# Kernel tuning notes

Hardware: AMD Instinct MI355X
Metric: run time of the kernel (lower is better)

Reference implementation:

```python
import jax, jax.numpy as jnp
import numpy as np

N_NODES = 50000
N_EDGES = 600000
D_IN = 128
D_HID = 128


def _sage_conv(x, src, dst, W_l, b_l, W_r):
    """PyG SAGEConv (mean aggr): out = lin_l(mean_{j in N(i)} x_j) + lin_r(x_i).
    bias lives in lin_l only."""
    n = x.shape[0]
    agg = jax.ops.segment_sum(x[src], dst, num_segments=n)            # [N, D]
    cnt = jax.ops.segment_sum(jnp.ones((src.shape[0],), x.dtype), dst, num_segments=n)
    mean = agg / jnp.maximum(cnt, 1.0)[:, None]
    return mean @ W_l.T + b_l + x @ W_r.T


def setup_inputs() -> dict:
    key = jax.random.key(0)
    ks = jax.random.split(key, 8)
    glorot = lambda k, o, i: jax.random.normal(k, (o, i), jnp.float32) * np.sqrt(2.0 / (o + i))
    return {
        "x": jax.random.normal(ks[0], (N_NODES, D_IN), jnp.float32),
        "edge_index": jax.random.randint(ks[1], (2, N_EDGES), 0, N_NODES, jnp.int64),
        "W1_l": glorot(ks[2], D_HID, D_IN),
        "b1": jnp.zeros((D_HID,), jnp.float32),
        "W1_r": glorot(ks[3], D_HID, D_IN),
        "W2_l": glorot(ks[4], D_HID, D_HID),
        "b2": jnp.zeros((D_HID,), jnp.float32),
        "W2_r": glorot(ks[5], D_HID, D_HID),
    }


def reference(x, edge_index, W1_l, b1, W1_r, W2_l, b2, W2_r):
    src, dst = edge_index[0], edge_index[1]
    h = _sage_conv(x, src, dst, W1_l, b1, W1_r)
    h = jax.nn.leaky_relu(h, negative_slope=0.2)
    return _sage_conv(h, src, dst, W2_l, b2, W2_r)
```

## Files before the change

kernel.cpp:

```cpp
#include <hip/hip_runtime.h>

#define N_NODES 50000
#define N_EDGES 600000
#define D 128
#define SCAN_BLOCKS ((N_NODES + 255) / 256)

typedef __attribute__((ext_vector_type(8))) short bf16x8;
typedef __attribute__((ext_vector_type(4))) float floatx4;

__device__ inline unsigned int f2bf(float f) {
    unsigned int u = __float_as_uint(f);
    return (u + 0x7FFFu + ((u >> 16) & 1u)) >> 16;
}
__device__ inline float bf_lo(unsigned int u) { return __uint_as_float(u << 16); }
__device__ inline float bf_hi(unsigned int u) { return __uint_as_float(u & 0xFFFF0000u); }

__global__ void k_prep(const float* __restrict__ x, unsigned short* __restrict__ xbf,
                       const float* __restrict__ wa, const float* __restrict__ wb,
                       const float* __restrict__ wc, const float* __restrict__ wd,
                       unsigned short* __restrict__ wbf,
                       const int* __restrict__ dst, int* __restrict__ cnt) {
    const int b = blockIdx.x;
    const int t = threadIdx.x;
    if (b < 6250) {
        int i = b * 256 + t;
        float4 v = ((const float4*)x)[i];
        uint2 o;
        o.x = f2bf(v.x) | (f2bf(v.y) << 16);
        o.y = f2bf(v.z) | (f2bf(v.w) << 16);
        ((uint2*)xbf)[i] = o;
    } else if (b < 6506) {
        int i = (b - 6250) * 256 + t;
        const float* srcs[4] = {wa, wb, wc, wd};
        wbf[i] = (unsigned short)f2bf(srcs[i >> 14][i & 16383]);
    } else {
        int e = (b - 6506) * 256 + t;
        if (e < N_EDGES) atomicAdd(&cnt[dst[e]], 1);
    }
}


__global__ void k_scan1(const int* __restrict__ cnt, int* __restrict__ off,
                        int* __restrict__ partial) {
    __shared__ int sdata[256];
    const int t = threadIdx.x;
    const int i = blockIdx.x * 256 + t;
    int v = (i < N_NODES) ? cnt[i] : 0;
    sdata[t] = v;
    __syncthreads();
    for (int d = 1; d < 256; d <<= 1) {
        int u = (t >= d) ? sdata[t - d] : 0;
        __syncthreads();
        sdata[t] += u;
        __syncthreads();
    }
    if (i < N_NODES) off[i] = sdata[t] - v;
    if (t == 255) partial[blockIdx.x] = sdata[255];
}

__global__ void k_scan2(int* __restrict__ partial) {
    __shared__ int sdata[256];
    const int t = threadIdx.x;
    int v = (t < SCAN_BLOCKS) ? partial[t] : 0;
    sdata[t] = v;
    __syncthreads();
    for (int d = 1; d < 256; d <<= 1) {
        int u = (t >= d) ? sdata[t - d] : 0;
        __syncthreads();
        sdata[t] += u;
        __syncthreads();
    }
    if (t < SCAN_BLOCKS) partial[t] = sdata[t] - v;
}

__global__ void k_scan3(int* __restrict__ off, const int* __restrict__ partial,
                        int* __restrict__ cursor) {
    const int i = blockIdx.x * 256 + threadIdx.x;
    if (i < N_NODES) {
        int o = off[i] + partial[blockIdx.x];
        off[i] = o;
        cursor[i] = o;
    }
    if (i == 0) off[N_NODES] = N_EDGES;
}

__global__ void k_bucket(const int* __restrict__ src, const int* __restrict__ dst,
                         int* __restrict__ cursor, int* __restrict__ ebuf) {
    int e = blockIdx.x * blockDim.x + threadIdx.x;
    if (e < N_EDGES) {
        int p = atomicAdd(&cursor[dst[e]], 1);
        ebuf[p] = src[e];
    }
}

template <bool RELU, bool OUT_BF16>
__global__ void __launch_bounds__(256) k_gather_layer(
    const int* __restrict__ off, const int* __restrict__ ebuf,
    const unsigned short* __restrict__ Xbf,
    const unsigned short* __restrict__ Wlbf, const float* __restrict__ bias,
    const unsigned short* __restrict__ Wrbf, void* __restrict__ outp) {
    __shared__ unsigned short tile[16][136];

    const int t = threadIdx.x;
    const int node0 = blockIdx.x * 16;

    {
        const int nl = t >> 4, q = t & 15;
        const int node = node0 + nl;
        int s0 = off[node], s1 = off[node + 1];
        float acc[8] = {0.f, 0.f, 0.f, 0.f, 0.f, 0.f, 0.f, 0.f};
        int e = s0;
        for (; e + 4 <= s1; e += 4) {
            int sa = ebuf[e], sb = ebuf[e + 1], sc = ebuf[e + 2], sd = ebuf[e + 3];
            uint4 va = *(const uint4*)(Xbf + (size_t)sa * D + q * 8);
            uint4 vb = *(const uint4*)(Xbf + (size_t)sb * D + q * 8);
            uint4 vc = *(const uint4*)(Xbf + (size_t)sc * D + q * 8);
            uint4 vd = *(const uint4*)(Xbf + (size_t)sd * D + q * 8);
            acc[0] += bf_lo(va.x) + bf_lo(vb.x) + bf_lo(vc.x) + bf_lo(vd.x);
            acc[1] += bf_hi(va.x) + bf_hi(vb.x) + bf_hi(vc.x) + bf_hi(vd.x);
            acc[2] += bf_lo(va.y) + bf_lo(vb.y) + bf_lo(vc.y) + bf_lo(vd.y);
            acc[3] += bf_hi(va.y) + bf_hi(vb.y) + bf_hi(vc.y) + bf_hi(vd.y);
            acc[4] += bf_lo(va.z) + bf_lo(vb.z) + bf_lo(vc.z) + bf_lo(vd.z);
            acc[5] += bf_hi(va.z) + bf_hi(vb.z) + bf_hi(vc.z) + bf_hi(vd.z);
            acc[6] += bf_lo(va.w) + bf_lo(vb.w) + bf_lo(vc.w) + bf_lo(vd.w);
            acc[7] += bf_hi(va.w) + bf_hi(vb.w) + bf_hi(vc.w) + bf_hi(vd.w);
        }
        for (; e < s1; ++e) {
            int sa = ebuf[e];
            uint4 va = *(const uint4*)(Xbf + (size_t)sa * D + q * 8);
            acc[0] += bf_lo(va.x); acc[1] += bf_hi(va.x);
            acc[2] += bf_lo(va.y); acc[3] += bf_hi(va.y);
            acc[4] += bf_lo(va.z); acc[5] += bf_hi(va.z);
            acc[6] += bf_lo(va.w); acc[7] += bf_hi(va.w);
        }
        float inv = (s1 > s0) ? 1.0f / (float)(s1 - s0) : 0.0f;
        uint4 o;
        o.x = f2bf(acc[0] * inv) | (f2bf(acc[1] * inv) << 16);
        o.y = f2bf(acc[2] * inv) | (f2bf(acc[3] * inv) << 16);
        o.z = f2bf(acc[4] * inv) | (f2bf(acc[5] * inv) << 16);
        o.w = f2bf(acc[6] * inv) | (f2bf(acc[7] * inv) << 16);
        *(uint4*)(&tile[nl][q * 8]) = o;
    }
    __syncthreads();

    const int lane = t & 63;
    const int wv = t >> 6;
    const int l15 = lane & 15;
    const int quad = lane >> 4;

    floatx4 c0 = (floatx4)(0.f), c1 = (floatx4)(0.f);
    const int nf0 = wv * 2, nf1 = wv * 2 + 1;

    const unsigned short* mrow = &tile[l15][quad * 8];
    const unsigned short* arowX = Xbf + (size_t)(node0 + l15) * D + quad * 8;

#pragma unroll
    for (int kk = 0; kk < 4; ++kk) {
        bf16x8 a = *(const bf16x8*)(mrow + kk * 32);
        bf16x8 b0 = *(const bf16x8*)(Wlbf + (size_t)(nf0 * 16 + l15) * D + kk * 32 + quad * 8);
        bf16x8 b1 = *(const bf16x8*)(Wlbf + (size_t)(nf1 * 16 + l15) * D + kk * 32 + quad * 8);
        c0 = __builtin_amdgcn_mfma_f32_16x16x32_bf16(a, b0, c0, 0, 0, 0);
        c1 = __builtin_amdgcn_mfma_f32_16x16x32_bf16(a, b1, c1, 0, 0, 0);
    }
#pragma unroll
    for (int kk = 0; kk < 4; ++kk) {
        bf16x8 a = *(const bf16x8*)(arowX + kk * 32);
        bf16x8 b0 = *(const bf16x8*)(Wrbf + (size_t)(nf0 * 16 + l15) * D + kk * 32 + quad * 8);
        bf16x8 b1 = *(const bf16x8*)(Wrbf + (size_t)(nf1 * 16 + l15) * D + kk * 32 + quad * 8);
        c0 = __builtin_amdgcn_mfma_f32_16x16x32_bf16(a, b0, c0, 0, 0, 0);
        c1 = __builtin_amdgcn_mfma_f32_16x16x32_bf16(a, b1, c1, 0, 0, 0);
    }

#pragma unroll
    for (int j = 0; j < 2; ++j) {
        floatx4 c = j ? c1 : c0;
        int f = (wv * 2 + j) * 16 + l15;
        float bv = bias[f];
#pragma unroll
        for (int r = 0; r < 4; ++r) {
            float v = c[r] + bv;
            if (RELU) v = v > 0.f ? v : 0.2f * v;
            int node = node0 + quad * 4 + r;
            if (OUT_BF16)
                ((unsigned short*)outp)[(size_t)node * D + f] = (unsigned short)f2bf(v);
            else
                ((float*)outp)[(size_t)node * D + f] = v;
        }
    }
}


extern "C" void kernel_launch(void* const* d_in, const int* in_sizes, int n_in,
                              void* d_out, int out_size, void* d_ws, size_t ws_size,
                              hipStream_t stream) {
    (void)in_sizes; (void)n_in; (void)out_size; (void)ws_size;

    const float* x   = (const float*)d_in[0];
    const int*   ei  = (const int*)d_in[1];
    const float* W1l = (const float*)d_in[2];
    const float* b1  = (const float*)d_in[3];
    const float* W1r = (const float*)d_in[4];
    const float* W2l = (const float*)d_in[5];
    const float* b2  = (const float*)d_in[6];
    const float* W2r = (const float*)d_in[7];

    const int* src = ei;
    const int* dst = ei + N_EDGES;

    char* ws = (char*)d_ws;
    int*   cnt     = (int*)(ws + 0);
    int*   off     = (int*)(ws + 200064);
    int*   cursor  = (int*)(ws + 400128);
    int*   partial = (int*)(ws + 600192);
    int*   ebuf    = (int*)(ws + 601216);
    unsigned short* wbf = (unsigned short*)(ws + 3001216);
    unsigned short* xbf = (unsigned short*)(ws + 3132288);
    unsigned short* hbf = (unsigned short*)(ws + 15932288);
    float* out = (float*)d_out;

    unsigned short* w1l_bf = wbf;
    unsigned short* w1r_bf = wbf + 16384;
    unsigned short* w2l_bf = wbf + 32768;
    unsigned short* w2r_bf = wbf + 49152;

    hipMemsetAsync(cnt, 0, N_NODES * sizeof(int), stream);
    k_prep<<<8850, 256, 0, stream>>>(x, xbf, W1l, W1r, W2l, W2r, wbf, dst, cnt);
    k_scan1<<<SCAN_BLOCKS, 256, 0, stream>>>(cnt, off, partial);
    k_scan2<<<1, 256, 0, stream>>>(partial);
    k_scan3<<<SCAN_BLOCKS, 256, 0, stream>>>(off, partial, cursor);
    k_bucket<<<(N_EDGES + 255) / 256, 256, 0, stream>>>(src, dst, cursor, ebuf);

    k_gather_layer<true, true><<<N_NODES / 16, 256, 0, stream>>>(
        off, ebuf, xbf, w1l_bf, b1, w1r_bf, (void*)hbf);
    k_gather_layer<false, false><<<N_NODES / 16, 256, 0, stream>>>(
        off, ebuf, hbf, w2l_bf, b2, w2r_bf, (void*)out);
}
```

Before: 251.8 us.

## Replace CSR scan/bucket build with fixed-capacity per-node neighbor lists

Drops the three scan kernels and the bucket kernel. The prep kernel now does a single atomic pass per edge that places each source id into a per-node slot array of capacity 64, stored as 16-bit indices. Edges past the capacity go to a global spill list, which the gather kernel scans linearly only for overflowing nodes. The gather loop is unrolled to 8 loads in flight, and the bf16 copy of x now lives in the output buffer to save workspace. This removes several kernel launches and the serial scan dependency. In exchange it relies on node ids fitting in 16 bits, and the spill path would be slow if many nodes had high degree.

```diff
diff --git a/kernel.cpp b/kernel.cpp
--- a/kernel.cpp
+++ b/kernel.cpp
@@ -3,7 +3,7 @@
 #define N_NODES 50000
 #define N_EDGES 600000
 #define D 128
-#define SCAN_BLOCKS ((N_NODES + 255) / 256)
+#define CAP 64
 
 typedef __attribute__((ext_vector_type(8))) short bf16x8;
 typedef __attribute__((ext_vector_type(4))) float floatx4;
@@ -19,83 +19,49 @@
                        const float* __restrict__ wa, const float* __restrict__ wb,
                        const float* __restrict__ wc, const float* __restrict__ wd,
                        unsigned short* __restrict__ wbf,
-                       const int* __restrict__ dst, int* __restrict__ cnt) {
+                       const int* __restrict__ src, const int* __restrict__ dst,
+                       int* __restrict__ cnt, unsigned short* __restrict__ buf,
+                       int* __restrict__ spillN, int* __restrict__ spillD,
+                       int* __restrict__ spillS) {
     const int b = blockIdx.x;
     const int t = threadIdx.x;
-    if (b < 6250) {
-        int i = b * 256 + t;
+    if (b < 2344) {
+        int e = b * 256 + t;
+        if (e < N_EDGES) {
+            int d = dst[e], s = src[e];
+            int p = atomicAdd(&cnt[d], 1);
+            if (p < CAP) {
+                buf[(size_t)d * CAP + p] = (unsigned short)s;
+            } else {
+                int k = atomicAdd(spillN, 1);
+                spillD[k] = d; spillS[k] = s;
+            }
+        }
+    } else if (b < 8594) {
+        int i = (b - 2344) * 256 + t;
         float4 v = ((const float4*)x)[i];
         uint2 o;
         o.x = f2bf(v.x) | (f2bf(v.y) << 16);
         o.y = f2bf(v.z) | (f2bf(v.w) << 16);
         ((uint2*)xbf)[i] = o;
-    } else if (b < 6506) {
-        int i = (b - 6250) * 256 + t;
+    } else {
+        int i = (b - 8594) * 256 + t;
         const float* srcs[4] = {wa, wb, wc, wd};
         wbf[i] = (unsigned short)f2bf(srcs[i >> 14][i & 16383]);
-    } else {
-        int e = (b - 6506) * 256 + t;
-        if (e < N_EDGES) atomicAdd(&cnt[dst[e]], 1);
-    }
-}
-
-
-__global__ void k_scan1(const int* __restrict__ cnt, int* __restrict__ off,
-                        int* __restrict__ partial) {
-    __shared__ int sdata[256];
-    const int t = threadIdx.x;
-    const int i = blockIdx.x * 256 + t;
-    int v = (i < N_NODES) ? cnt[i] : 0;
-    sdata[t] = v;
-    __syncthreads();
-    for (int d = 1; d < 256; d <<= 1) {
-        int u = (t >= d) ? sdata[t - d] : 0;
-        __syncthreads();
-        sdata[t] += u;
-        __syncthreads();
-    }
-    if (i < N_NODES) off[i] = sdata[t] - v;
-    if (t == 255) partial[blockIdx.x] = sdata[255];
-}
-
-__global__ void k_scan2(int* __restrict__ partial) {
-    __shared__ int sdata[256];
-    const int t = threadIdx.x;
-    int v = (t < SCAN_BLOCKS) ? partial[t] : 0;
-    sdata[t] = v;
-    __syncthreads();
-    for (int d = 1; d < 256; d <<= 1) {
-        int u = (t >= d) ? sdata[t - d] : 0;
-        __syncthreads();
-        sdata[t] += u;
-        __syncthreads();
-    }
-    if (t < SCAN_BLOCKS) partial[t] = sdata[t] - v;
-}
-
-__global__ void k_scan3(int* __restrict__ off, const int* __restrict__ partial,
-                        int* __restrict__ cursor) {
-    const int i = blockIdx.x * 256 + threadIdx.x;
-    if (i < N_NODES) {
-        int o = off[i] + partial[blockIdx.x];
-        off[i] = o;
-        cursor[i] = o;
-    }
-    if (i == 0) off[N_NODES] = N_EDGES;
-}
-
-__global__ void k_bucket(const int* __restrict__ src, const int* __restrict__ dst,
-                         int* __restrict__ cursor, int* __restrict__ ebuf) {
-    int e = blockIdx.x * blockDim.x + threadIdx.x;
-    if (e < N_EDGES) {
-        int p = atomicAdd(&cursor[dst[e]], 1);
-        ebuf[p] = src[e];
-    }
-}
+    }
+}
+
+#define ACC8(vv) do { \
+    acc[0] += bf_lo((vv).x); acc[1] += bf_hi((vv).x); \
+    acc[2] += bf_lo((vv).y); acc[3] += bf_hi((vv).y); \
+    acc[4] += bf_lo((vv).z); acc[5] += bf_hi((vv).z); \
+    acc[6] += bf_lo((vv).w); acc[7] += bf_hi((vv).w); } while (0)
 
 template <bool RELU, bool OUT_BF16>
 __global__ void __launch_bounds__(256) k_gather_layer(
-    const int* __restrict__ off, const int* __restrict__ ebuf,
+    const int* __restrict__ cnt, const unsigned short* __restrict__ buf,
+    const int* __restrict__ spillN, const int* __restrict__ spillD,
+    const int* __restrict__ spillS,
     const unsigned short* __restrict__ Xbf,
     const unsigned short* __restrict__ Wlbf, const float* __restrict__ bias,
     const unsigned short* __restrict__ Wrbf, void* __restrict__ outp) {
@@ -107,33 +73,41 @@
     {
         const int nl = t >> 4, q = t & 15;
         const int node = node0 + nl;
-        int s0 = off[node], s1 = off[node + 1];
+        const int deg = cnt[node];
+        const int m = deg < CAP ? deg : CAP;
+        const unsigned short* __restrict__ nb = buf + (size_t)node * CAP;
         float acc[8] = {0.f, 0.f, 0.f, 0.f, 0.f, 0.f, 0.f, 0.f};
-        int e = s0;
-        for (; e + 4 <= s1; e += 4) {
-            int sa = ebuf[e], sb = ebuf[e + 1], sc = ebuf[e + 2], sd = ebuf[e + 3];
-            uint4 va = *(const uint4*)(Xbf + (size_t)sa * D + q * 8);
-            uint4 vb = *(const uint4*)(Xbf + (size_t)sb * D + q * 8);
-            uint4 vc = *(const uint4*)(Xbf + (size_t)sc * D + q * 8);
-            uint4 vd = *(const uint4*)(Xbf + (size_t)sd * D + q * 8);
-            acc[0] += bf_lo(va.x) + bf_lo(vb.x) + bf_lo(vc.x) + bf_lo(vd.x);
-            acc[1] += bf_hi(va.x) + bf_hi(vb.x) + bf_hi(vc.x) + bf_hi(vd.x);
-            acc[2] += bf_lo(va.y) + bf_lo(vb.y) + bf_lo(vc.y) + bf_lo(vd.y);
-            acc[3] += bf_hi(va.y) + bf_hi(vb.y) + bf_hi(vc.y) + bf_hi(vd.y);
-            acc[4] += bf_lo(va.z) + bf_lo(vb.z) + bf_lo(vc.z) + bf_lo(vd.z);
-            acc[5] += bf_hi(va.z) + bf_hi(vb.z) + bf_hi(vc.z) + bf_hi(vd.z);
-            acc[6] += bf_lo(va.w) + bf_lo(vb.w) + bf_lo(vc.w) + bf_lo(vd.w);
-            acc[7] += bf_hi(va.w) + bf_hi(vb.w) + bf_hi(vc.w) + bf_hi(vd.w);
-        }
-        for (; e < s1; ++e) {
-            int sa = ebuf[e];
-            uint4 va = *(const uint4*)(Xbf + (size_t)sa * D + q * 8);
-            acc[0] += bf_lo(va.x); acc[1] += bf_hi(va.x);
-            acc[2] += bf_lo(va.y); acc[3] += bf_hi(va.y);
-            acc[4] += bf_lo(va.z); acc[5] += bf_hi(va.z);
-            acc[6] += bf_lo(va.w); acc[7] += bf_hi(va.w);
-        }
-        float inv = (s1 > s0) ? 1.0f / (float)(s1 - s0) : 0.0f;
+        int e = 0;
+        for (; e + 8 <= m; e += 8) {
+            uint4 v[8];
+#pragma unroll
+            for (int u = 0; u < 8; ++u)
+                v[u] = *(const uint4*)(Xbf + (size_t)nb[e + u] * D + q * 8);
+#pragma unroll
+            for (int u = 0; u < 8; ++u) ACC8(v[u]);
+        }
+        for (; e + 4 <= m; e += 4) {
+            uint4 v[4];
+#pragma unroll
+            for (int u = 0; u < 4; ++u)
+                v[u] = *(const uint4*)(Xbf + (size_t)nb[e + u] * D + q * 8);
+#pragma unroll
+            for (int u = 0; u < 4; ++u) ACC8(v[u]);
+        }
+        for (; e < m; ++e) {
+            uint4 v = *(const uint4*)(Xbf + (size_t)nb[e] * D + q * 8);
+            ACC8(v);
+        }
+        if (deg > CAP) {
+            int sn = *spillN;
+            for (int k = 0; k < sn; ++k) {
+                if (spillD[k] == node) {
+                    uint4 v = *(const uint4*)(Xbf + (size_t)spillS[k] * D + q * 8);
+                    ACC8(v);
+                }
+            }
+        }
+        float inv = (deg > 0) ? 1.0f / (float)deg : 0.0f;
         uint4 o;
         o.x = f2bf(acc[0] * inv) | (f2bf(acc[1] * inv) << 16);
         o.y = f2bf(acc[2] * inv) | (f2bf(acc[3] * inv) << 16);
@@ -208,14 +182,15 @@
     const int* dst = ei + N_EDGES;
 
     char* ws = (char*)d_ws;
-    int*   cnt     = (int*)(ws + 0);
-    int*   off     = (int*)(ws + 200064);
-    int*   cursor  = (int*)(ws + 400128);
-    int*   partial = (int*)(ws + 600192);
-    int*   ebuf    = (int*)(ws + 601216);
-    unsigned short* wbf = (unsigned short*)(ws + 3001216);
-    unsigned short* xbf = (unsigned short*)(ws + 3132288);
-    unsigned short* hbf = (unsigned short*)(ws + 15932288);
+    int* cnt              = (int*)(ws + 0);
+    int* spillN           = (int*)(ws + 200000);
+    int* spillD           = (int*)(ws + 200064);
+    int* spillS           = (int*)(ws + 2600064);
+    unsigned short* buf   = (unsigned short*)(ws + 5000064);
+    unsigned short* wbf   = (unsigned short*)(ws + 11400064);
+    unsigned short* hbf   = (unsigned short*)(ws + 11531136);
+
+    unsigned short* xbf = (unsigned short*)d_out;
     float* out = (float*)d_out;
 
     unsigned short* w1l_bf = wbf;
@@ -223,15 +198,13 @@
     unsigned short* w2l_bf = wbf + 32768;
     unsigned short* w2r_bf = wbf + 49152;
 
-    hipMemsetAsync(cnt, 0, N_NODES * sizeof(int), stream);
-    k_prep<<<8850, 256, 0, stream>>>(x, xbf, W1l, W1r, W2l, W2r, wbf, dst, cnt);
-    k_scan1<<<SCAN_BLOCKS, 256, 0, stream>>>(cnt, off, partial);
-    k_scan2<<<1, 256, 0, stream>>>(partial);
-    k_scan3<<<SCAN_BLOCKS, 256, 0, stream>>>(off, partial, cursor);
-    k_bucket<<<(N_EDGES + 255) / 256, 256, 0, stream>>>(src, dst, cursor, ebuf);
+    hipMemsetAsync(ws, 0, 200064, stream);
+
+    k_prep<<<8850, 256, 0, stream>>>(x, xbf, W1l, W1r, W2l, W2r, wbf,
+                                     src, dst, cnt, buf, spillN, spillD, spillS);
 
     k_gather_layer<true, true><<<N_NODES / 16, 256, 0, stream>>>(
-        off, ebuf, xbf, w1l_bf, b1, w1r_bf, (void*)hbf);
+        cnt, buf, spillN, spillD, spillS, xbf, w1l_bf, b1, w1r_bf, (void*)hbf);
     k_gather_layer<false, false><<<N_NODES / 16, 256, 0, stream>>>(
-        off, ebuf, hbf, w2l_bf, b2, w2r_bf, (void*)out);
-}
+        cnt, buf, spillN, spillD, spillS, hbf, w2l_bf, b2, w2r_bf, (void*)out);
+}
```

New measurement: 223.7 us. 11.2% less time.
